# Performance work log

Measured on AMD Instinct MI355X. Metric: run time of the kernel, lower is better.

The kernel has to match this reference:

```python
import jax, jax.numpy as jnp
import numpy as np

DIM = 384
HEADS = 12
W = 7  # window_size
N = W * W
B = 4096

def _relative_position_index(ws):
    ch = np.arange(ws)
    coords = np.stack(np.meshgrid(ch, ch, indexing='ij'))  # [2, W, W]
    cf = coords.reshape(2, -1)  # [2, W*W]
    rel = cf[:, :, None] - cf[:, None, :]  # [2, N, N]
    rel = rel.transpose(1, 2, 0)
    rel[:, :, 0] += ws - 1
    rel[:, :, 1] += ws - 1
    rel[:, :, 0] *= 2 * ws - 1
    return rel.sum(-1).astype(np.int32)  # [N, N]

def setup_inputs() -> dict:
    key = jax.random.key(0)
    ks = jax.random.split(key, 8)
    s = 0.02
    return {
        'x': jax.random.normal(ks[0], (B, N, DIM), jnp.float32),
        'y': jax.random.normal(ks[1], (B, N, DIM), jnp.float32),
        'q_w': jax.random.normal(ks[2], (DIM, DIM), jnp.float32) * s,
        'q_b': jnp.zeros((DIM,), jnp.float32),
        'kv_w': jax.random.normal(ks[3], (2 * DIM, DIM), jnp.float32) * s,
        'kv_b': jnp.zeros((2 * DIM,), jnp.float32),
        'proj_w': jax.random.normal(ks[4], (DIM, DIM), jnp.float32) * s,
        'proj_b': jnp.zeros((DIM,), jnp.float32),
        'rel_table': jax.random.normal(ks[5], ((2 * W - 1) ** 2, HEADS), jnp.float32) * s,
        'rel_index': jnp.asarray(_relative_position_index(W)),
    }

def reference(x, y, q_w, q_b, kv_w, kv_b, proj_w, proj_b, rel_table, rel_index):
    Bx, N1, C = x.shape
    N2 = y.shape[1]
    hd = C // HEADS
    scale = hd ** -0.5
    # projections (torch Linear: x @ W^T + b)
    q = (x @ q_w.T + q_b).reshape(Bx, N1, HEADS, hd)
    kv = (y @ kv_w.T + kv_b).reshape(Bx, N2, 2, HEADS, hd)
    k = kv[:, :, 0]  # [B, N2, H, d]
    v = kv[:, :, 1]
    attn = jnp.einsum('bqhd,bkhd->bhqk', q, k) * scale
    # relative position bias: [N1, N2, H] -> [H, N1, N2]
    bias = rel_table[rel_index.reshape(-1)].reshape(N1, N2, HEADS)
    attn = attn + jnp.transpose(bias, (2, 0, 1))[None]
    attn = jax.nn.softmax(attn, axis=-1)
    out = jnp.einsum('bhqk,bkhd->bqhd', attn, v).reshape(Bx, N1, C)
    return out @ proj_w.T + proj_b
```

## Files before the change

kernel.cpp:

```cpp
#include <hip/hip_runtime.h>

#define DIM 384
#define HEADS 12
#define HD 32
#define NTOK 49
#define NWIN 4096
#define MTOT (NWIN*NTOK)
#define PSTR 72

typedef __attribute__((ext_vector_type(8))) __bf16 bf16x8;
typedef __attribute__((ext_vector_type(4))) __bf16 bf16x4;
typedef __attribute__((ext_vector_type(4))) float f32x4;

static __device__ __forceinline__ f32x4 mfma16(bf16x8 a, bf16x8 b, f32x4 c) {
  return __builtin_amdgcn_mfma_f32_16x16x32_bf16(a, b, c, 0, 0, 0);
}

static __device__ __forceinline__ void gload_lds16(const void* g, void* l) {
  __builtin_amdgcn_global_load_lds(
      (const __attribute__((address_space(1))) unsigned int*)g,
      (__attribute__((address_space(3))) unsigned int*)l, 16, 0, 0);
}

static __device__ __forceinline__ bf16x4 cvt4(float4 v) {
  bf16x4 t;
  t[0]=(__bf16)v.x; t[1]=(__bf16)v.y; t[2]=(__bf16)v.z; t[3]=(__bf16)v.w;
  return t;
}

__global__ void k_prep(const float* __restrict__ qw, const float* __restrict__ kvw,
                       const float* __restrict__ pw, const float* __restrict__ rel_table,
                       const int* __restrict__ rel_index,
                       __bf16* __restrict__ qw_bf, __bf16* __restrict__ kvw_bf,
                       __bf16* __restrict__ pw_bf, float* __restrict__ bias_pad) {
  int i = blockIdx.x * 256 + threadIdx.x;
  if (i < DIM*DIM)   qw_bf[i] = (__bf16)qw[i];
  if (i < 2*DIM*DIM) kvw_bf[i] = (__bf16)kvw[i];
  if (i < DIM*DIM)   pw_bf[i] = (__bf16)pw[i];
  if (i < HEADS*64*64) {
    int h = i >> 12, rem = i & 4095, q = rem >> 6, k = rem & 63;
    float v;
    if (k >= NTOK)      v = -1e30f;
    else if (q >= NTOK) v = 0.0f;
    else v = rel_table[rel_index[q*NTOK + k] * HEADS + h];
    bias_pad[i] = v;
  }
}

__global__ __launch_bounds__(256, 4) void k_qkv(
    const float* __restrict__ x, const float* __restrict__ y,
    const __bf16* __restrict__ qw_bf, const __bf16* __restrict__ kvw_bf,
    const float* __restrict__ q_b, const float* __restrict__ kv_b,
    __bf16* __restrict__ Qws, __bf16* __restrict__ Kws, __bf16* __restrict__ Vws)
{
  int b = blockIdx.x;
  int orig = (b & 7) * 1764 + (b >> 3);
  int mtile = orig / 9;
  int nt9 = orig - mtile*9;
  const float* A; const __bf16* Bw; const float* bias; __bf16* Cout;
  int wrow0, col0;
  if (nt9 < 3) { A = x; Bw = qw_bf; bias = q_b; Cout = Qws; wrow0 = nt9*128; col0 = wrow0; }
  else {
    A = y; Bw = kvw_bf; bias = kv_b; wrow0 = (nt9-3)*128;
    if (wrow0 < DIM) { Cout = Kws; col0 = wrow0; } else { Cout = Vws; col0 = wrow0 - DIM; }
  }
  bias += wrow0;

  __shared__ __align__(16) __bf16 As[2][128*32];
  __shared__ __align__(16) __bf16 Bs[2][128*32];

  int t = threadIdx.x, lane = t & 63, wave = t >> 6;
  int l15 = lane & 15, g = lane >> 4;
  int wr = (wave >> 1) * 64, wc = (wave & 1) * 64;
  int row0b = mtile*128;

  int c8 = lane & 7;
  int r8 = lane >> 3;
  int swk = (lane >> 4) & 3;
  const float* asrc = A + (size_t)(row0b + wave*32 + r8)*DIM + c8*4;
  unsigned lwb = (unsigned)wave*2048 + (unsigned)r8*64
               + ((((c8 >> 1) ^ swk) << 4) + (c8 & 1)*8);

  int sr  = 2*(lane >> 3) + ((lane >> 2) & 1);
  int scb = (lane & 3) ^ ((lane >> 3) & 3);
  const __bf16* bsrc[2];
  #pragma unroll
  for (int j = 0; j < 2; ++j)
    bsrc[j] = Bw + (size_t)(wrow0 + (wave*2 + j)*16 + sr)*DIM + scb*8;

  f32x4 acc[4][4];
  #pragma unroll
  for (int a=0;a<4;a++)
    #pragma unroll
    for (int bb=0;bb<4;bb++) acc[a][bb] = (f32x4){0.f,0.f,0.f,0.f};

  float4 r0, r1, r2, r3;
  r0 = *(const float4*)(asrc);
  r1 = *(const float4*)(asrc +  8*DIM);
  r2 = *(const float4*)(asrc + 16*DIM);
  r3 = *(const float4*)(asrc + 24*DIM);
  #pragma unroll
  for (int j = 0; j < 2; ++j)
    gload_lds16(bsrc[j], (char*)&Bs[0][0] + (wave*2+j)*1024);
  *(bf16x4*)((char*)&As[0][0] + lwb +    0) = cvt4(r0);
  *(bf16x4*)((char*)&As[0][0] + lwb +  512) = cvt4(r1);
  *(bf16x4*)((char*)&As[0][0] + lwb + 1024) = cvt4(r2);
  *(bf16x4*)((char*)&As[0][0] + lwb + 1536) = cvt4(r3);
  __syncthreads();

  int lslot = l15*64 + ((g ^ ((l15 >> 1) & 3)) << 4);

  int buf = 0;
  #pragma unroll 2
  for (int kt = 0; kt < 12; ++kt) {
    if (kt < 11) {
      int kk = (kt+1)*32;
      r0 = *(const float4*)(asrc + kk);
      r1 = *(const float4*)(asrc + kk +  8*DIM);
      r2 = *(const float4*)(asrc + kk + 16*DIM);
      r3 = *(const float4*)(asrc + kk + 24*DIM);
      #pragma unroll
      for (int j = 0; j < 2; ++j)
        gload_lds16(bsrc[j] + kk, (char*)&Bs[buf^1][0] + (wave*2+j)*1024);
    }
    bf16x8 af[4], bfv[4];
    #pragma unroll
    for (int a=0;a<4;a++)
      af[a]  = *(const bf16x8*)((const char*)&As[buf][0] + (wr + a*16)*64 + lslot);
    #pragma unroll
    for (int bb=0;bb<4;bb++)
      bfv[bb] = *(const bf16x8*)((const char*)&Bs[buf][0] + (wc + bb*16)*64 + lslot);
    #pragma unroll
    for (int a=0;a<4;a++)
      #pragma unroll
      for (int bb=0;bb<4;bb++)
        acc[a][bb] = mfma16(af[a], bfv[bb], acc[a][bb]);
    if (kt < 11) {
      *(bf16x4*)((char*)&As[buf^1][0] + lwb +    0) = cvt4(r0);
      *(bf16x4*)((char*)&As[buf^1][0] + lwb +  512) = cvt4(r1);
      *(bf16x4*)((char*)&As[buf^1][0] + lwb + 1024) = cvt4(r2);
      *(bf16x4*)((char*)&As[buf^1][0] + lwb + 1536) = cvt4(r3);
    }
    __syncthreads();
    buf ^= 1;
  }

  #pragma unroll
  for (int a=0;a<4;a++) {
    #pragma unroll
    for (int bb=0;bb<4;bb++) {
      int colw = wc + bb*16 + l15;
      float bi = bias[colw];
      size_t cbase = (size_t)(row0b + wr + a*16 + 4*g)*DIM + (col0 + colw);
      #pragma unroll
      for (int r=0;r<4;r++)
        Cout[cbase + (size_t)r*DIM] = (__bf16)(acc[a][bb][r] + bi);
    }
  }
}

__global__ __launch_bounds__(256) void k_attn(
    __bf16* qao,
    const __bf16* __restrict__ Kws, const __bf16* __restrict__ Vws,
    const float* __restrict__ bias_pad)
{
  __shared__ __align__(16) __bf16 Psh[4][64*PSTR];
  __shared__ __align__(16) __bf16 VTsh[4][32*PSTR];
  int b = blockIdx.x;
  int lane = threadIdx.x & 63, wave = threadIdx.x >> 6;
  int l15 = lane & 15, g = lane >> 4;
  __bf16* Pw  = Psh[wave];
  __bf16* VTw = VTsh[wave];
  size_t rowbase = (size_t)b * NTOK * DIM;
  const float scale = 0.17677669529663687f;

  for (int e = lane; e < 32*15; e += 64) {
    int d = e / 15, k = 49 + (e - d*15);
    VTw[d*PSTR + k] = (__bf16)0.0f;
  }

  for (int hh = 0; hh < 3; hh++) {
    int h = wave + hh*4;
    for (int e = lane; e < NTOK*HD; e += 64) {
      int k = e >> 5, d = e & 31;
      VTw[d*PSTR + k] = Vws[rowbase + (size_t)k*DIM + h*HD + d];
    }
    bf16x8 qf[4], kf[4];
    #pragma unroll
    for (int mt=0; mt<4; mt++) {
      int q = 16*mt + l15; if (q > 48) q = 48;
      qf[mt] = *(const bf16x8*)(qao + rowbase + (size_t)q*DIM + h*HD + g*8);
    }
    #pragma unroll
    for (int nt=0; nt<4; nt++) {
      int kk = 16*nt + l15; if (kk > 48) kk = 48;
      kf[nt] = *(const bf16x8*)(Kws + rowbase + (size_t)kk*DIM + h*HD + g*8);
    }
    f32x4 sacc[4][4];
    #pragma unroll
    for (int mt=0; mt<4; mt++)
      #pragma unroll
      for (int nt=0; nt<4; nt++)
        sacc[mt][nt] = mfma16(qf[mt], kf[nt], (f32x4){0.f,0.f,0.f,0.f});

    const float* bt = bias_pad + h*4096;
    float rs[4][4];
    #pragma unroll
    for (int mt=0; mt<4; mt++) {
      #pragma unroll
      for (int r=0; r<4; r++) {
        int q = 16*mt + 4*g + r;
        float v0 = sacc[mt][0][r]*scale + bt[q*64 +  0 + l15];
        float v1 = sacc[mt][1][r]*scale + bt[q*64 + 16 + l15];
        float v2 = sacc[mt][2][r]*scale + bt[q*64 + 32 + l15];
        float v3 = sacc[mt][3][r]*scale + bt[q*64 + 48 + l15];
        float m = fmaxf(fmaxf(v0,v1), fmaxf(v2,v3));
        #pragma unroll
        for (int off=1; off<16; off<<=1) m = fmaxf(m, __shfl_xor(m, off));
        v0 = __expf(v0-m); v1 = __expf(v1-m); v2 = __expf(v2-m); v3 = __expf(v3-m);
        float s = v0+v1+v2+v3;
        #pragma unroll
        for (int off=1; off<16; off<<=1) s += __shfl_xor(s, off);
        rs[mt][r] = s;
        Pw[q*PSTR +  0 + l15] = (__bf16)v0;
        Pw[q*PSTR + 16 + l15] = (__bf16)v1;
        Pw[q*PSTR + 32 + l15] = (__bf16)v2;
        Pw[q*PSTR + 48 + l15] = (__bf16)v3;
      }
    }

    #pragma unroll
    for (int mt=0; mt<4; mt++) {
      #pragma unroll
      for (int dt=0; dt<2; dt++) {
        f32x4 o = (f32x4){0.f,0.f,0.f,0.f};
        #pragma unroll
        for (int ks=0; ks<2; ks++) {
          bf16x8 pa = *(const bf16x8*)(Pw  + (16*mt + l15)*PSTR + 32*ks + 8*g);
          bf16x8 vb = *(const bf16x8*)(VTw + (16*dt + l15)*PSTR + 32*ks + 8*g);
          o = mfma16(pa, vb, o);
        }
        #pragma unroll
        for (int r=0; r<4; r++) {
          int q = 16*mt + 4*g + r;
          if (q < NTOK)
            qao[rowbase + (size_t)q*DIM + h*HD + 16*dt + l15] = (__bf16)(o[r] / rs[mt][r]);
        }
      }
    }
  }
}

__global__ __launch_bounds__(256, 4) void k_proj(
    const __bf16* __restrict__ Aao, const __bf16* __restrict__ pw_bf,
    const float* __restrict__ pb, float* __restrict__ out)
{
  int b = blockIdx.x;
  int orig = (b & 7) * 588 + (b >> 3);
  int mtile = orig / 3;
  int nt = orig - mtile*3;
  int lane = threadIdx.x & 63, wave = threadIdx.x >> 6;
  int l15 = lane & 15, g = lane >> 4;
  int wr = (wave >> 1) * 64, wc = (wave & 1) * 64;
  int row0b = mtile*128;
  int col00 = nt*128;

  __shared__ __align__(16) __bf16 As[2][128*32];
  __shared__ __align__(16) __bf16 Bs[2][128*32];

  int sr  = 2*(lane >> 3) + ((lane >> 2) & 1);
  int scb = (lane & 3) ^ ((lane >> 3) & 3);
  const __bf16* asrc[2]; const __bf16* bsrc[2];
  #pragma unroll
  for (int j = 0; j < 2; ++j) {
    int ar = (wave*2 + j)*16 + sr;
    asrc[j] = Aao   + (size_t)(row0b + ar)*DIM + scb*8;
    bsrc[j] = pw_bf + (size_t)(col00 + ar)*DIM + scb*8;
  }

  f32x4 acc[4][4];
  #pragma unroll
  for (int a=0;a<4;a++)
    #pragma unroll
    for (int bb=0;bb<4;bb++) acc[a][bb] = (f32x4){0.f,0.f,0.f,0.f};

  #pragma unroll
  for (int j = 0; j < 2; ++j) {
    gload_lds16(asrc[j], (char*)&As[0][0] + (wave*2+j)*1024);
    gload_lds16(bsrc[j], (char*)&Bs[0][0] + (wave*2+j)*1024);
  }
  __syncthreads();

  int lslot = l15*64 + ((g ^ ((l15 >> 1) & 3)) << 4);

  int buf = 0;
  #pragma unroll 2
  for (int kt = 0; kt < 12; ++kt) {
    if (kt < 11) {
      int kk = (kt+1)*32;
      #pragma unroll
      for (int j = 0; j < 2; ++j) {
        gload_lds16(asrc[j] + kk, (char*)&As[buf^1][0] + (wave*2+j)*1024);
        gload_lds16(bsrc[j] + kk, (char*)&Bs[buf^1][0] + (wave*2+j)*1024);
      }
    }
    bf16x8 af[4], bfv[4];
    #pragma unroll
    for (int a=0;a<4;a++)
      af[a]  = *(const bf16x8*)((const char*)&As[buf][0] + (wr + a*16)*64 + lslot);
    #pragma unroll
    for (int bb=0;bb<4;bb++)
      bfv[bb] = *(const bf16x8*)((const char*)&Bs[buf][0] + (wc + bb*16)*64 + lslot);
    #pragma unroll
    for (int a=0;a<4;a++)
      #pragma unroll
      for (int bb=0;bb<4;bb++)
        acc[a][bb] = mfma16(af[a], bfv[bb], acc[a][bb]);
    __syncthreads();
    buf ^= 1;
  }

  #pragma unroll
  for (int a=0;a<4;a++) {
    #pragma unroll
    for (int bb=0;bb<4;bb++) {
      int col = col00 + wc + bb*16 + l15;
      float bi = pb[col];
      size_t cbase = (size_t)(row0b + wr + a*16 + 4*g)*DIM + col;
      #pragma unroll
      for (int r=0;r<4;r++)
        out[cbase + (size_t)r*DIM] = acc[a][bb][r] + bi;
    }
  }
}

extern "C" void kernel_launch(void* const* d_in, const int* in_sizes, int n_in,
                              void* d_out, int out_size, void* d_ws, size_t ws_size,
                              hipStream_t stream)
{
  const float* x   = (const float*)d_in[0];
  const float* y   = (const float*)d_in[1];
  const float* qw  = (const float*)d_in[2];
  const float* qb  = (const float*)d_in[3];
  const float* kvw = (const float*)d_in[4];
  const float* kvb = (const float*)d_in[5];
  const float* pw  = (const float*)d_in[6];
  const float* pb  = (const float*)d_in[7];
  const float* rt  = (const float*)d_in[8];
  const int*   ri  = (const int*)d_in[9];
  float* out = (float*)d_out;

  char* ws = (char*)d_ws;
  const size_t WS_NEEDED = 1376256ull + 3ull*154140672ull;
  if (ws_size < WS_NEEDED) return;

  __bf16* qw_bf    = (__bf16*)(ws);
  __bf16* kvw_bf   = (__bf16*)(ws + 294912);
  __bf16* pw_bf    = (__bf16*)(ws + 884736);
  float*  bias_pad = (float*)(ws + 1179648);
  __bf16* Qws      = (__bf16*)(ws + 1376256);
  __bf16* Kws      = Qws + (size_t)MTOT*DIM;
  __bf16* Vws      = Kws + (size_t)MTOT*DIM;

  k_prep<<<dim3(1152), dim3(256), 0, stream>>>(qw, kvw, pw, rt, ri, qw_bf, kvw_bf, pw_bf, bias_pad);
  k_qkv <<<dim3(1568*9), dim3(256), 0, stream>>>(x, y, qw_bf, kvw_bf, qb, kvb, Qws, Kws, Vws);
  k_attn<<<dim3(NWIN), dim3(256), 0, stream>>>(Qws, Kws, Vws, bias_pad);
  k_proj<<<dim3(1568*3), dim3(256), 0, stream>>>(Qws, pw_bf, pb, out);
}
```

Before: 846.0 us.

## Triple-buffer LDS weight tiles with prefetch distance two in projection GEMMs

```diff
diff --git a/kernel.cpp b/kernel.cpp
--- a/kernel.cpp
+++ b/kernel.cpp
@@ -66,8 +66,8 @@
   }
   bias += wrow0;
 
-  __shared__ __align__(16) __bf16 As[2][128*32];
-  __shared__ __align__(16) __bf16 Bs[2][128*32];
+  __shared__ __align__(16) __bf16 As[2*128*32];
+  __shared__ __align__(16) __bf16 Bs[3*128*32];
 
   int t = threadIdx.x, lane = t & 63, wave = t >> 6;
   int l15 = lane & 15, g = lane >> 4;
@@ -83,10 +83,8 @@
 
   int sr  = 2*(lane >> 3) + ((lane >> 2) & 1);
   int scb = (lane & 3) ^ ((lane >> 3) & 3);
-  const __bf16* bsrc[2];
-  #pragma unroll
-  for (int j = 0; j < 2; ++j)
-    bsrc[j] = Bw + (size_t)(wrow0 + (wave*2 + j)*16 + sr)*DIM + scb*8;
+  const __bf16* bsrc0 = Bw + (size_t)(wrow0 + (wave*2    )*16 + sr)*DIM + scb*8;
+  const __bf16* bsrc1 = Bw + (size_t)(wrow0 + (wave*2 + 1)*16 + sr)*DIM + scb*8;
 
   f32x4 acc[4][4];
   #pragma unroll
@@ -94,55 +92,65 @@
     #pragma unroll
     for (int bb=0;bb<4;bb++) acc[a][bb] = (f32x4){0.f,0.f,0.f,0.f};
 
-  float4 r0, r1, r2, r3;
-  r0 = *(const float4*)(asrc);
-  r1 = *(const float4*)(asrc +  8*DIM);
-  r2 = *(const float4*)(asrc + 16*DIM);
-  r3 = *(const float4*)(asrc + 24*DIM);
-  #pragma unroll
-  for (int j = 0; j < 2; ++j)
-    gload_lds16(bsrc[j], (char*)&Bs[0][0] + (wave*2+j)*1024);
-  *(bf16x4*)((char*)&As[0][0] + lwb +    0) = cvt4(r0);
-  *(bf16x4*)((char*)&As[0][0] + lwb +  512) = cvt4(r1);
-  *(bf16x4*)((char*)&As[0][0] + lwb + 1024) = cvt4(r2);
-  *(bf16x4*)((char*)&As[0][0] + lwb + 1536) = cvt4(r3);
-  __syncthreads();
+  {
+    float4 s0 = *(const float4*)(asrc);
+    float4 s1 = *(const float4*)(asrc +  8*DIM);
+    float4 s2 = *(const float4*)(asrc + 16*DIM);
+    float4 s3 = *(const float4*)(asrc + 24*DIM);
+    gload_lds16(bsrc0,      (char*)Bs +        (wave*2  )*1024);
+    gload_lds16(bsrc1,      (char*)Bs +        (wave*2+1)*1024);
+    gload_lds16(bsrc0 + 32, (char*)Bs + 8192 + (wave*2  )*1024);
+    gload_lds16(bsrc1 + 32, (char*)Bs + 8192 + (wave*2+1)*1024);
+    *(bf16x4*)((char*)As + lwb +    0) = cvt4(s0);
+    *(bf16x4*)((char*)As + lwb +  512) = cvt4(s1);
+    *(bf16x4*)((char*)As + lwb + 1024) = cvt4(s2);
+    *(bf16x4*)((char*)As + lwb + 1536) = cvt4(s3);
+    asm volatile("s_waitcnt vmcnt(2)" ::: "memory");
+    asm volatile("s_waitcnt lgkmcnt(0)" ::: "memory");
+    __builtin_amdgcn_s_barrier();
+  }
 
   int lslot = l15*64 + ((g ^ ((l15 >> 1) & 3)) << 4);
 
-  int buf = 0;
-  #pragma unroll 2
+  #pragma unroll
   for (int kt = 0; kt < 12; ++kt) {
+    const int cur2 = kt & 1, nxt2 = cur2 ^ 1;
+    const int cur3 = kt % 3, pre3 = (kt + 2) % 3;
+    float4 s0, s1, s2, s3;
     if (kt < 11) {
-      int kk = (kt+1)*32;
-      r0 = *(const float4*)(asrc + kk);
-      r1 = *(const float4*)(asrc + kk +  8*DIM);
-      r2 = *(const float4*)(asrc + kk + 16*DIM);
-      r3 = *(const float4*)(asrc + kk + 24*DIM);
-      #pragma unroll
-      for (int j = 0; j < 2; ++j)
-        gload_lds16(bsrc[j] + kk, (char*)&Bs[buf^1][0] + (wave*2+j)*1024);
+      int kk = (kt + 1) * 32;
+      s0 = *(const float4*)(asrc + kk);
+      s1 = *(const float4*)(asrc + kk +  8*DIM);
+      s2 = *(const float4*)(asrc + kk + 16*DIM);
+      s3 = *(const float4*)(asrc + kk + 24*DIM);
+    }
+    if (kt < 10) {
+      int kk = (kt + 2) * 32;
+      gload_lds16(bsrc0 + kk, (char*)Bs + pre3*8192 + (wave*2  )*1024);
+      gload_lds16(bsrc1 + kk, (char*)Bs + pre3*8192 + (wave*2+1)*1024);
     }
     bf16x8 af[4], bfv[4];
     #pragma unroll
     for (int a=0;a<4;a++)
-      af[a]  = *(const bf16x8*)((const char*)&As[buf][0] + (wr + a*16)*64 + lslot);
+      af[a]  = *(const bf16x8*)((const char*)As + cur2*8192 + (wr + a*16)*64 + lslot);
     #pragma unroll
     for (int bb=0;bb<4;bb++)
-      bfv[bb] = *(const bf16x8*)((const char*)&Bs[buf][0] + (wc + bb*16)*64 + lslot);
+      bfv[bb] = *(const bf16x8*)((const char*)Bs + cur3*8192 + (wc + bb*16)*64 + lslot);
     #pragma unroll
     for (int a=0;a<4;a++)
       #pragma unroll
       for (int bb=0;bb<4;bb++)
         acc[a][bb] = mfma16(af[a], bfv[bb], acc[a][bb]);
     if (kt < 11) {
-      *(bf16x4*)((char*)&As[buf^1][0] + lwb +    0) = cvt4(r0);
-      *(bf16x4*)((char*)&As[buf^1][0] + lwb +  512) = cvt4(r1);
-      *(bf16x4*)((char*)&As[buf^1][0] + lwb + 1024) = cvt4(r2);
-      *(bf16x4*)((char*)&As[buf^1][0] + lwb + 1536) = cvt4(r3);
-    }
-    __syncthreads();
-    buf ^= 1;
+      *(bf16x4*)((char*)As + nxt2*8192 + lwb +    0) = cvt4(s0);
+      *(bf16x4*)((char*)As + nxt2*8192 + lwb +  512) = cvt4(s1);
+      *(bf16x4*)((char*)As + nxt2*8192 + lwb + 1024) = cvt4(s2);
+      *(bf16x4*)((char*)As + nxt2*8192 + lwb + 1536) = cvt4(s3);
+      if (kt < 10) asm volatile("s_waitcnt vmcnt(2)" ::: "memory");
+      else         asm volatile("s_waitcnt vmcnt(0)" ::: "memory");
+      asm volatile("s_waitcnt lgkmcnt(0)" ::: "memory");
+      __builtin_amdgcn_s_barrier();
+    }
   }
 
   #pragma unroll
@@ -265,18 +273,15 @@
   int row0b = mtile*128;
   int col00 = nt*128;
 
-  __shared__ __align__(16) __bf16 As[2][128*32];
-  __shared__ __align__(16) __bf16 Bs[2][128*32];
+  __shared__ __align__(16) __bf16 As[3*128*32];
+  __shared__ __align__(16) __bf16 Bs[3*128*32];
 
   int sr  = 2*(lane >> 3) + ((lane >> 2) & 1);
   int scb = (lane & 3) ^ ((lane >> 3) & 3);
-  const __bf16* asrc[2]; const __bf16* bsrc[2];
-  #pragma unroll
-  for (int j = 0; j < 2; ++j) {
-    int ar = (wave*2 + j)*16 + sr;
-    asrc[j] = Aao   + (size_t)(row0b + ar)*DIM + scb*8;
-    bsrc[j] = pw_bf + (size_t)(col00 + ar)*DIM + scb*8;
-  }
+  const __bf16* asrc0 = Aao   + (size_t)(row0b + (wave*2    )*16 + sr)*DIM + scb*8;
+  const __bf16* asrc1 = Aao   + (size_t)(row0b + (wave*2 + 1)*16 + sr)*DIM + scb*8;
+  const __bf16* bsrc0 = pw_bf + (size_t)(col00 + (wave*2    )*16 + sr)*DIM + scb*8;
+  const __bf16* bsrc1 = pw_bf + (size_t)(col00 + (wave*2 + 1)*16 + sr)*DIM + scb*8;
 
   f32x4 acc[4][4];
   #pragma unroll
@@ -284,40 +289,48 @@
     #pragma unroll
     for (int bb=0;bb<4;bb++) acc[a][bb] = (f32x4){0.f,0.f,0.f,0.f};
 
-  #pragma unroll
-  for (int j = 0; j < 2; ++j) {
-    gload_lds16(asrc[j], (char*)&As[0][0] + (wave*2+j)*1024);
-    gload_lds16(bsrc[j], (char*)&Bs[0][0] + (wave*2+j)*1024);
-  }
-  __syncthreads();
+  {
+    gload_lds16(asrc0,      (char*)As +        (wave*2  )*1024);
+    gload_lds16(asrc1,      (char*)As +        (wave*2+1)*1024);
+    gload_lds16(bsrc0,      (char*)Bs +        (wave*2  )*1024);
+    gload_lds16(bsrc1,      (char*)Bs +        (wave*2+1)*1024);
+    gload_lds16(asrc0 + 32, (char*)As + 8192 + (wave*2  )*1024);
+    gload_lds16(asrc1 + 32, (char*)As + 8192 + (wave*2+1)*1024);
+    gload_lds16(bsrc0 + 32, (char*)Bs + 8192 + (wave*2  )*1024);
+    gload_lds16(bsrc1 + 32, (char*)Bs + 8192 + (wave*2+1)*1024);
+    asm volatile("s_waitcnt vmcnt(4)" ::: "memory");
+    __builtin_amdgcn_s_barrier();
+  }
 
   int lslot = l15*64 + ((g ^ ((l15 >> 1) & 3)) << 4);
 
-  int buf = 0;
-  #pragma unroll 2
+  #pragma unroll
   for (int kt = 0; kt < 12; ++kt) {
-    if (kt < 11) {
-      int kk = (kt+1)*32;
-      #pragma unroll
-      for (int j = 0; j < 2; ++j) {
-        gload_lds16(asrc[j] + kk, (char*)&As[buf^1][0] + (wave*2+j)*1024);
-        gload_lds16(bsrc[j] + kk, (char*)&Bs[buf^1][0] + (wave*2+j)*1024);
-      }
+    const int cur3 = kt % 3, pre3 = (kt + 2) % 3;
+    if (kt < 10) {
+      int kk = (kt + 2) * 32;
+      gload_lds16(asrc0 + kk, (char*)As + pre3*8192 + (wave*2  )*1024);
+      gload_lds16(asrc1 + kk, (char*)As + pre3*8192 + (wave*2+1)*1024);
+      gload_lds16(bsrc0 + kk, (char*)Bs + pre3*8192 + (wave*2  )*1024);
+      gload_lds16(bsrc1 + kk, (char*)Bs + pre3*8192 + (wave*2+1)*1024);
     }
     bf16x8 af[4], bfv[4];
     #pragma unroll
     for (int a=0;a<4;a++)
-      af[a]  = *(const bf16x8*)((const char*)&As[buf][0] + (wr + a*16)*64 + lslot);
+      af[a]  = *(const bf16x8*)((const char*)As + cur3*8192 + (wr + a*16)*64 + lslot);
     #pragma unroll
     for (int bb=0;bb<4;bb++)
-      bfv[bb] = *(const bf16x8*)((const char*)&Bs[buf][0] + (wc + bb*16)*64 + lslot);
+      bfv[bb] = *(const bf16x8*)((const char*)Bs + cur3*8192 + (wc + bb*16)*64 + lslot);
     #pragma unroll
     for (int a=0;a<4;a++)
       #pragma unroll
       for (int bb=0;bb<4;bb++)
         acc[a][bb] = mfma16(af[a], bfv[bb], acc[a][bb]);
-    __syncthreads();
-    buf ^= 1;
+    if (kt < 11) {
+      if (kt < 10) asm volatile("s_waitcnt vmcnt(4)" ::: "memory");
+      else         asm volatile("s_waitcnt vmcnt(0)" ::: "memory");
+      __builtin_amdgcn_s_barrier();
+    }
   }
 
   #pragma unroll
```

Result: no change. 840.8 us (-0.6%).
